# Optimization experiments

Measured on AMD Instinct MI355X. Metric: run time of the kernel, lower is better.

Reference implementation:

```python
import jax, jax.numpy as jnp
import numpy as np

M, N = 128, 128          # SOM grid
NITER = 1000             # total training iterations
ALPHA = 0.3              # base learning rate (torch default)
SIGMA = max(M, N) / 2.0  # base neighbourhood radius (torch default)
BS, DIM = 4096, 768


def setup_inputs() -> dict:
    key = jax.random.key(0)
    k1, k2 = jax.random.split(key)
    embedded = jax.random.normal(k1, (BS, DIM), dtype=jnp.float32)   # SapBERT CLS reps
    weights = jax.random.normal(k2, (M * N, DIM), dtype=jnp.float32)  # codebook / SOM weights
    return {"embedded": embedded, "weights": weights, "it": 100}


def reference(embedded, weights, it):
    comps = weights.shape[0]
    # neuron grid locations [comps, 2] (row-major i,j like neuron_locations())
    locs = jnp.stack(
        jnp.meshgrid(jnp.arange(M), jnp.arange(N), indexing="ij"), axis=-1
    ).reshape(comps, 2).astype(jnp.float32)

    # BMU search: squared Euclidean distances (argmin identical to argmin of sqrt)
    # [bs, comps] — avoids materializing the torch [bs, comps, dim] repeat
    d2 = (
        jnp.sum(embedded * embedded, axis=1)[:, None]
        + jnp.sum(weights * weights, axis=1)[None, :]
        - 2.0 * (embedded @ weights.T)
    )
    bmu_index = jnp.argmin(d2, axis=1)          # [bs]
    bmu_loc = locs[bmu_index]                   # [bs, 2] gather

    # linearly decaying learning rate / sigma
    decay = 1.0 - it / NITER
    alpha_op = ALPHA * decay
    sigma_op = SIGMA * decay

    # Gaussian neighbourhood over grid distances [bs, comps]
    grid_d2 = jnp.sum((locs[None, :, :] - bmu_loc[:, None, :]) ** 2, axis=-1)
    lr = alpha_op * jnp.exp(-grid_d2 / (sigma_op * sigma_op))

    # delta[c,d] = sum_b lr[b,c] * (x[b,d] - w[c,d])  (no bs x comps x dim materialization)
    delta = jnp.einsum("bc,bd->cd", lr, embedded) - jnp.sum(lr, axis=0)[:, None] * weights
    return weights + delta
```

## Files before the change

### kernel.cpp

```cpp
#include <hip/hip_runtime.h>
#include <cstdint>
#include <cstddef>

#define BS    4096
#define DIM   768
#define GM    128
#define GN    128
#define COMPS (GM * GN)
#define NITER_F 1000.0f
#define ALPHA0  0.3f
#define SIGMA0  64.0f

typedef _Float16 half8  __attribute__((ext_vector_type(8)));
typedef _Float16 half4v __attribute__((ext_vector_type(4)));
typedef _Float16 half2v __attribute__((ext_vector_type(2)));
typedef float    floatx4 __attribute__((ext_vector_type(4)));

#define XH_OFF    0UL
#define WH_OFF    (8UL * 1024UL * 1024UL)
#define G_OFF     0UL
#define G_BYTES   ((size_t)COMPS * DIM * 4UL)
#define BEST_OFF  G_BYTES
#define BEST_BYTES ((size_t)BS * 8UL)
#define CNT_OFF   (BEST_OFF + BEST_BYTES)
#define CNT_BYTES ((size_t)COMPS * 4UL)
#define CNTH_OFF  (CNT_OFF + CNT_BYTES)
#define S_OFF     (CNTH_OFF + CNT_BYTES)
#define WN2_OFF   (S_OFF + CNT_BYTES)

#define GPTR(p) ((const __attribute__((address_space(1))) void*)(p))
#define LPTR(p) ((__attribute__((address_space(3))) void*)(p))

__device__ __forceinline__ unsigned long long packScore(float s, int c) {
    unsigned u = __float_as_uint(s);
    u = (u & 0x80000000u) ? ~u : (u | 0x80000000u);
    return ((unsigned long long)u << 32) | (unsigned)(~(unsigned)c);
}

__device__ __forceinline__ unsigned long long shfl_xor_u64(unsigned long long v, int m) {
    unsigned lo = (unsigned)v, hi = (unsigned)(v >> 32);
    lo = (unsigned)__shfl_xor((int)lo, m, 64);
    hi = (unsigned)__shfl_xor((int)hi, m, 64);
    return ((unsigned long long)hi << 32) | lo;
}

__global__ void cvt_kernel(const float* __restrict__ src, _Float16* __restrict__ dst, int n4) {
    int i = blockIdx.x * 256 + threadIdx.x;
    if (i >= n4) return;
    float4 v = ((const float4*)src)[i];
    half4v h;
    h[0] = (_Float16)v.x; h[1] = (_Float16)v.y;
    h[2] = (_Float16)v.z; h[3] = (_Float16)v.w;
    ((half4v*)dst)[i] = h;
}

__global__ __launch_bounds__(192) void cvtw_wn2_kernel(
    const float* __restrict__ w, _Float16* __restrict__ wh, float* __restrict__ wn2) {
    const int c = blockIdx.x;
    const int t = threadIdx.x;
    const size_t i4 = (size_t)c * 192 + t;
    float4 v = ((const float4*)w)[i4];
    half4v h;
    h[0] = (_Float16)v.x; h[1] = (_Float16)v.y;
    h[2] = (_Float16)v.z; h[3] = (_Float16)v.w;
    ((half4v*)wh)[i4] = h;
    float s = v.x * v.x + v.y * v.y + v.z * v.z + v.w * v.w;
    #pragma unroll
    for (int off = 32; off; off >>= 1) s += __shfl_down(s, off, 64);
    __shared__ float p[3];
    if ((t & 63) == 0) p[t >> 6] = s;
    __syncthreads();
    if (t == 0) wn2[c] = 0.5f * (p[0] + p[1] + p[2]);
}

__global__ __launch_bounds__(256) void bmu_kernel(
    const _Float16* __restrict__ xh, const _Float16* __restrict__ wh,
    const float* __restrict__ wn2, unsigned long long* __restrict__ best) {
    __shared__ _Float16 xs[128 * 32];
    __shared__ _Float16 wsd[128 * 32];
    __shared__ unsigned long long red[128];

    const int tid  = threadIdx.x;
    const int wv   = tid >> 6;
    const int lane = tid & 63;
    const int c0 = blockIdx.x * 128;
    const int b0 = blockIdx.y * 128;

    if (tid < 128) red[tid] = 0ULL;

    floatx4 acc[4][4];
    #pragma unroll
    for (int i = 0; i < 4; ++i)
        #pragma unroll
        for (int j = 0; j < 4; ++j) acc[i][j] = (floatx4){0.f, 0.f, 0.f, 0.f};

    const int rr   = lane >> 2;
    const int pq   = lane & 3;
    const int kk   = pq ^ ((rr >> 1) & 3);
    const int lk   = kk * 8;
    const int q    = lane >> 4;
    const int l15  = lane & 15;
    const int mrow = (wv >> 1) * 64;
    const int ncol = (wv & 1) * 64;

    for (int k0 = 0; k0 < DIM; k0 += 32) {
        #pragma unroll
        for (int s = 0; s < 2; ++s) {
            const int sub = 2 * wv + s;
            const _Float16* gx = xh + (size_t)(b0 + sub * 16 + rr) * DIM + k0 + lk;
            __builtin_amdgcn_global_load_lds(GPTR(gx), LPTR(xs + sub * 512), 16, 0, 0);
            const _Float16* gw = wh + (size_t)(c0 + sub * 16 + rr) * DIM + k0 + lk;
            __builtin_amdgcn_global_load_lds(GPTR(gw), LPTR(wsd + sub * 512), 16, 0, 0);
        }
        __syncthreads();

        half8 af[4], bf[4];
        #pragma unroll
        for (int i = 0; i < 4; ++i) {
            const int row = mrow + i * 16 + l15;
            af[i] = *(const half8*)(xs + row * 32 + (q ^ ((row >> 1) & 3)) * 8);
        }
        #pragma unroll
        for (int j = 0; j < 4; ++j) {
            const int row = ncol + j * 16 + l15;
            bf[j] = *(const half8*)(wsd + row * 32 + (q ^ ((row >> 1) & 3)) * 8);
        }
        #pragma unroll
        for (int i = 0; i < 4; ++i)
            #pragma unroll
            for (int j = 0; j < 4; ++j)
                acc[i][j] = __builtin_amdgcn_mfma_f32_16x16x32_f16(af[i], bf[j], acc[i][j], 0, 0, 0);
        __syncthreads();
    }

    float wnj[4];
    #pragma unroll
    for (int j = 0; j < 4; ++j) wnj[j] = wn2[c0 + ncol + j * 16 + l15];

    #pragma unroll
    for (int i = 0; i < 4; ++i) {
        #pragma unroll
        for (int r = 0; r < 4; ++r) {
            unsigned long long m = 0ULL;
            #pragma unroll
            for (int j = 0; j < 4; ++j) {
                float s = acc[i][j][r] - wnj[j];
                unsigned long long p = packScore(s, c0 + ncol + j * 16 + l15);
                if (p > m) m = p;
            }
            #pragma unroll
            for (int msk = 1; msk <= 8; msk <<= 1) {
                unsigned long long o = shfl_xor_u64(m, msk);
                if (o > m) m = o;
            }
            if (l15 == 0)
                atomicMax(&red[mrow + i * 16 + q * 4 + r], m);
        }
    }
    __syncthreads();
    if (tid < 128) atomicMax(&best[b0 + tid], red[tid]);
}

__global__ void scatter_kernel(const unsigned long long* __restrict__ best,
                               const float* __restrict__ x,
                               float* __restrict__ G, float* __restrict__ cnt) {
    const int b = blockIdx.x;
    const int c = (int)(~(unsigned)(best[b] & 0xFFFFFFFFULL));
    float* gr = G + (size_t)c * DIM;
    const float* xr = x + (size_t)b * DIM;
    #pragma unroll
    for (int u = 0; u < 3; ++u) {
        const int d = threadIdx.x + u * 256;
        atomicAdd(&gr[d], xr[d]);
    }
    if (threadIdx.x == 0) atomicAdd(&cnt[c], 1.0f);
}

#define EP 136
#define BP 40

__global__ __launch_bounds__(256) void convA_kernel(
    const float* __restrict__ G, float* __restrict__ H, const int* __restrict__ itp) {
    __shared__ _Float16 Es[128 * EP];
    __shared__ _Float16 Bs[128 * BP];
    const int d0 = blockIdx.x * 128;
    const int ib = blockIdx.y;
    const int tid = threadIdx.x;
    const int wv = tid >> 6, lane = tid & 63;
    const int l15 = lane & 15, q = lane >> 4;
    const int mrow = (wv >> 1) * 64, ncol = (wv & 1) * 64;

    {
        const float decay = 1.f - (float)(*itp) / NITER_F;
        const float sig = SIGMA0 * decay;
        const float inv = -1.f / (sig * sig);
        const int row = tid >> 1, hh = tid & 1;
        _Float16* dst = Es + row * EP + hh * 64;
        #pragma unroll
        for (int u = 0; u < 64; ++u) {
            const float dd = (float)(row - hh * 64 - u);
            dst[u] = (_Float16)__expf(dd * dd * inv);
        }
    }

    floatx4 acc[4][4];
    #pragma unroll
    for (int i = 0; i < 4; ++i)
        #pragma unroll
        for (int j = 0; j < 4; ++j) acc[i][j] = (floatx4){0.f, 0.f, 0.f, 0.f};

    const int jj2 = (tid & 15) * 2;
    const int dd  = (tid >> 4) * 8;
    for (int k0 = 0; k0 < 128; k0 += 32) {
        __syncthreads();
        {
            const float* r0 = G + (size_t)(ib * 128 + k0 + jj2) * DIM + d0 + dd;
            const float* r1 = r0 + DIM;
            float4 a0 = *(const float4*)r0, a1 = *(const float4*)(r0 + 4);
            float4 b0 = *(const float4*)r1, b1 = *(const float4*)(r1 + 4);
            float va[8] = {a0.x, a0.y, a0.z, a0.w, a1.x, a1.y, a1.z, a1.w};
            float vb[8] = {b0.x, b0.y, b0.z, b0.w, b1.x, b1.y, b1.z, b1.w};
            #pragma unroll
            for (int u = 0; u < 8; ++u)
                *(half2v*)(Bs + (dd + u) * BP + jj2) = (half2v){(_Float16)va[u], (_Float16)vb[u]};
        }
        __syncthreads();
        half8 af[4], bf[4];
        #pragma unroll
        for (int i = 0; i < 4; ++i)
            af[i] = *(const half8*)(Es + (mrow + i * 16 + l15) * EP + k0 + q * 8);
        #pragma unroll
        for (int j = 0; j < 4; ++j)
            bf[j] = *(const half8*)(Bs + (ncol + j * 16 + l15) * BP + q * 8);
        #pragma unroll
        for (int i = 0; i < 4; ++i)
            #pragma unroll
            for (int j = 0; j < 4; ++j)
                acc[i][j] = __builtin_amdgcn_mfma_f32_16x16x32_f16(af[i], bf[j], acc[i][j], 0, 0, 0);
    }
    __syncthreads();
    float* Ebf = (float*)Es;
    #pragma unroll
    for (int ch = 0; ch < 2; ++ch) {
        if ((wv >> 1) == ch) {
            #pragma unroll
            for (int i = 0; i < 4; ++i)
                #pragma unroll
                for (int j = 0; j < 4; ++j)
                    #pragma unroll
                    for (int r = 0; r < 4; ++r)
                        Ebf[(i * 16 + q * 4 + r) * 132 + ncol + j * 16 + l15] = acc[i][j][r];
        }
        __syncthreads();
        {
            const int row = tid >> 2, seg = tid & 3;
            const int m = ch * 64 + row;
            const size_t g = (size_t)(ib * 128 + m) * DIM + d0 + seg * 32;
            #pragma unroll
            for (int u = 0; u < 8; ++u)
                *(float4*)(H + g + u * 4) = *(const float4*)(Ebf + row * 132 + seg * 32 + u * 4);
        }
        __syncthreads();
    }
}

__global__ __launch_bounds__(256) void convB_kernel(
    const float* H, const float* __restrict__ w,
    const float* __restrict__ S, const int* __restrict__ itp, float* out) {
    __shared__ _Float16 Es[128 * EP];
    __shared__ _Float16 Bs[128 * BP];
    const int d0 = blockIdx.x * 128;
    const int jc = blockIdx.y;
    const int tid = threadIdx.x;
    const int wv = tid >> 6, lane = tid & 63;
    const int l15 = lane & 15, q = lane >> 4;
    const int mrow = (wv >> 1) * 64, ncol = (wv & 1) * 64;
    const float alpha = ALPHA0 * (1.f - (float)(*itp) / NITER_F);

    {
        const float decay = 1.f - (float)(*itp) / NITER_F;
        const float sig = SIGMA0 * decay;
        const float inv = -1.f / (sig * sig);
        const int row = tid >> 1, hh = tid & 1;
        _Float16* dst = Es + row * EP + hh * 64;
        #pragma unroll
        for (int u = 0; u < 64; ++u) {
            const float dd = (float)(row - hh * 64 - u);
            dst[u] = (_Float16)__expf(dd * dd * inv);
        }
    }

    floatx4 acc[4][4];
    #pragma unroll
    for (int i = 0; i < 4; ++i)
        #pragma unroll
        for (int j = 0; j < 4; ++j) acc[i][j] = (floatx4){0.f, 0.f, 0.f, 0.f};

    const int jj2 = (tid & 15) * 2;
    const int dd  = (tid >> 4) * 8;
    for (int k0 = 0; k0 < 128; k0 += 32) {
        __syncthreads();
        {
            const float* r0 = H + (size_t)((k0 + jj2) * 128 + jc) * DIM + d0 + dd;
            const float* r1 = r0 + (size_t)128 * DIM;
            float4 a0 = *(const float4*)r0, a1 = *(const float4*)(r0 + 4);
            float4 b0 = *(const float4*)r1, b1 = *(const float4*)(r1 + 4);
            float va[8] = {a0.x, a0.y, a0.z, a0.w, a1.x, a1.y, a1.z, a1.w};
            float vb[8] = {b0.x, b0.y, b0.z, b0.w, b1.x, b1.y, b1.z, b1.w};
            #pragma unroll
            for (int u = 0; u < 8; ++u)
                *(half2v*)(Bs + (dd + u) * BP + jj2) = (half2v){(_Float16)va[u], (_Float16)vb[u]};
        }
        __syncthreads();
        half8 af[4], bf[4];
        #pragma unroll
        for (int i = 0; i < 4; ++i)
            af[i] = *(const half8*)(Es + (mrow + i * 16 + l15) * EP + k0 + q * 8);
        #pragma unroll
        for (int j = 0; j < 4; ++j)
            bf[j] = *(const half8*)(Bs + (ncol + j * 16 + l15) * BP + q * 8);
        #pragma unroll
        for (int i = 0; i < 4; ++i)
            #pragma unroll
            for (int j = 0; j < 4; ++j)
                acc[i][j] = __builtin_amdgcn_mfma_f32_16x16x32_f16(af[i], bf[j], acc[i][j], 0, 0, 0);
    }
    __syncthreads();
    float* Ebf = (float*)Es;
    #pragma unroll
    for (int ch = 0; ch < 2; ++ch) {
        if ((wv >> 1) == ch) {
            #pragma unroll
            for (int i = 0; i < 4; ++i)
                #pragma unroll
                for (int j = 0; j < 4; ++j)
                    #pragma unroll
                    for (int r = 0; r < 4; ++r)
                        Ebf[(i * 16 + q * 4 + r) * 132 + ncol + j * 16 + l15] = acc[i][j][r];
        }
        __syncthreads();
        {
            const int row = tid >> 2, seg = tid & 3;
            const int m = ch * 64 + row;
            const int c = m * 128 + jc;
            const float scl = 1.f - alpha * S[c];
            const size_t g = (size_t)c * DIM + d0 + seg * 32;
            #pragma unroll
            for (int u = 0; u < 8; ++u) {
                float4 wv4 = *(const float4*)(w + g + u * 4);
                float4 t4  = *(const float4*)(Ebf + row * 132 + seg * 32 + u * 4);
                float4 o;
                o.x = wv4.x * scl + alpha * t4.x;
                o.y = wv4.y * scl + alpha * t4.y;
                o.z = wv4.z * scl + alpha * t4.z;
                o.w = wv4.w * scl + alpha * t4.w;
                *(float4*)(out + g + u * 4) = o;
            }
        }
        __syncthreads();
    }
}

__global__ void cntconv1(const float* __restrict__ cnt, float* __restrict__ cntH,
                         const int* __restrict__ itp) {
    const int idx = blockIdx.x * 256 + threadIdx.x;
    const int i = idx >> 7, jc = idx & 127;
    const float decay = 1.f - (float)(*itp) / NITER_F;
    const float sig = SIGMA0 * decay;
    const float inv = -1.f / (sig * sig);
    float s = 0.f;
    for (int j = 0; j < 128; ++j) {
        const float dd = (float)(jc - j);
        s += __expf(dd * dd * inv) * cnt[i * 128 + j];
    }
    cntH[idx] = s;
}
__global__ void cntconv2(const float* __restrict__ cntH, float* __restrict__ S,
                         const int* __restrict__ itp) {
    const int idx = blockIdx.x * 256 + threadIdx.x;
    const int ic = idx >> 7, jc = idx & 127;
    const float decay = 1.f - (float)(*itp) / NITER_F;
    const float sig = SIGMA0 * decay;
    const float inv = -1.f / (sig * sig);
    float s = 0.f;
    for (int i = 0; i < 128; ++i) {
        const float dd = (float)(ic - i);
        s += __expf(dd * dd * inv) * cntH[i * 128 + jc];
    }
    S[idx] = s;
}

extern "C" void kernel_launch(void* const* d_in, const int* in_sizes, int n_in,
                              void* d_out, int out_size, void* d_ws, size_t ws_size,
                              hipStream_t stream) {
    const float* x  = (const float*)d_in[0];
    const float* w  = (const float*)d_in[1];
    const int* itp  = (const int*)d_in[2];
    float* out = (float*)d_out;
    char* ws = (char*)d_ws;

    _Float16* xh = (_Float16*)(ws + XH_OFF);
    _Float16* wh = (_Float16*)(ws + WH_OFF);
    float*    G  = (float*)(ws + G_OFF);
    unsigned long long* best = (unsigned long long*)(ws + BEST_OFF);
    float* cnt  = (float*)(ws + CNT_OFF);
    float* cntH = (float*)(ws + CNTH_OFF);
    float* S    = (float*)(ws + S_OFF);
    float* wn2  = (float*)(ws + WN2_OFF);

    hipMemsetAsync(ws + BEST_OFF, 0, BEST_BYTES + CNT_BYTES, stream);

    cvt_kernel<<<(BS * DIM / 4 + 255) / 256, 256, 0, stream>>>(x, xh, BS * DIM / 4);
    cvtw_wn2_kernel<<<COMPS, 192, 0, stream>>>(w, wh, wn2);

    bmu_kernel<<<dim3(COMPS / 128, BS / 128), 256, 0, stream>>>(xh, wh, wn2, best);

    hipMemsetAsync(ws + G_OFF, 0, G_BYTES, stream);
    scatter_kernel<<<BS, 256, 0, stream>>>(best, x, G, cnt);

    cntconv1<<<COMPS / 256, 256, 0, stream>>>(cnt, cntH, itp);
    cntconv2<<<COMPS / 256, 256, 0, stream>>>(cntH, S, itp);

    convA_kernel<<<dim3(6, 128), 256, 0, stream>>>(G, out, itp);
    convB_kernel<<<dim3(6, 128), 256, 0, stream>>>(out, w, S, itp, out);
}
```

Before: 346.9 us.

## Widen BMU K-tile, store intermediate as fp16 in-place, fuse count convolutions into convB

The BMU GEMM now stages 64-wide K tiles with an 8-way XOR swizzle, which halves the number of barrier pairs. convA writes its intermediate H as fp16 into the G buffer, interleaved per row, instead of fp32 into the output, cutting that traffic roughly in half. The two separable count-convolution kernels are removed, and each convB block now computes its 128 S values in shared memory. The cost is redundant exp work in every convB block (each of the 768 blocks recomputes its column's count convolution) and a risk of the in-place fp16 H overwriting G rows that another block still reads.

```diff
diff --git a/kernel.cpp b/kernel.cpp
--- a/kernel.cpp
+++ b/kernel.cpp
@@ -13,7 +13,6 @@
 
 typedef _Float16 half8  __attribute__((ext_vector_type(8)));
 typedef _Float16 half4v __attribute__((ext_vector_type(4)));
-typedef _Float16 half2v __attribute__((ext_vector_type(2)));
 typedef float    floatx4 __attribute__((ext_vector_type(4)));
 
 #define XH_OFF    0UL
@@ -24,9 +23,7 @@
 #define BEST_BYTES ((size_t)BS * 8UL)
 #define CNT_OFF   (BEST_OFF + BEST_BYTES)
 #define CNT_BYTES ((size_t)COMPS * 4UL)
-#define CNTH_OFF  (CNT_OFF + CNT_BYTES)
-#define S_OFF     (CNTH_OFF + CNT_BYTES)
-#define WN2_OFF   (S_OFF + CNT_BYTES)
+#define WN2_OFF   (CNT_OFF + CNT_BYTES)
 
 #define GPTR(p) ((const __attribute__((address_space(1))) void*)(p))
 #define LPTR(p) ((__attribute__((address_space(3))) void*)(p))
@@ -76,8 +73,8 @@
 __global__ __launch_bounds__(256) void bmu_kernel(
     const _Float16* __restrict__ xh, const _Float16* __restrict__ wh,
     const float* __restrict__ wn2, unsigned long long* __restrict__ best) {
-    __shared__ _Float16 xs[128 * 32];
-    __shared__ _Float16 wsd[128 * 32];
+    __shared__ _Float16 xs[128 * 64];
+    __shared__ _Float16 wsd[128 * 64];
     __shared__ unsigned long long red[128];
 
     const int tid  = threadIdx.x;
@@ -94,42 +91,47 @@
         #pragma unroll
         for (int j = 0; j < 4; ++j) acc[i][j] = (floatx4){0.f, 0.f, 0.f, 0.f};
 
-    const int rr   = lane >> 2;
-    const int pq   = lane & 3;
-    const int kk   = pq ^ ((rr >> 1) & 3);
-    const int lk   = kk * 8;
+    const int srow = lane >> 3;
+    const int spos = lane & 7;
     const int q    = lane >> 4;
     const int l15  = lane & 15;
     const int mrow = (wv >> 1) * 64;
     const int ncol = (wv & 1) * 64;
 
-    for (int k0 = 0; k0 < DIM; k0 += 32) {
-        #pragma unroll
-        for (int s = 0; s < 2; ++s) {
-            const int sub = 2 * wv + s;
-            const _Float16* gx = xh + (size_t)(b0 + sub * 16 + rr) * DIM + k0 + lk;
-            __builtin_amdgcn_global_load_lds(GPTR(gx), LPTR(xs + sub * 512), 16, 0, 0);
-            const _Float16* gw = wh + (size_t)(c0 + sub * 16 + rr) * DIM + k0 + lk;
-            __builtin_amdgcn_global_load_lds(GPTR(gw), LPTR(wsd + sub * 512), 16, 0, 0);
-        }
-        __syncthreads();
-
-        half8 af[4], bf[4];
-        #pragma unroll
-        for (int i = 0; i < 4; ++i) {
-            const int row = mrow + i * 16 + l15;
-            af[i] = *(const half8*)(xs + row * 32 + (q ^ ((row >> 1) & 3)) * 8);
-        }
-        #pragma unroll
-        for (int j = 0; j < 4; ++j) {
-            const int row = ncol + j * 16 + l15;
-            bf[j] = *(const half8*)(wsd + row * 32 + (q ^ ((row >> 1) & 3)) * 8);
-        }
-        #pragma unroll
-        for (int i = 0; i < 4; ++i)
-            #pragma unroll
-            for (int j = 0; j < 4; ++j)
-                acc[i][j] = __builtin_amdgcn_mfma_f32_16x16x32_f16(af[i], bf[j], acc[i][j], 0, 0, 0);
+    for (int k0 = 0; k0 < DIM; k0 += 64) {
+        #pragma unroll
+        for (int s = 0; s < 4; ++s) {
+            const int rbase = wv * 32 + s * 8;
+            const int row = rbase + srow;
+            const int kk = spos ^ (row & 7);
+            const _Float16* gx = xh + (size_t)(b0 + row) * DIM + k0 + kk * 8;
+            __builtin_amdgcn_global_load_lds(GPTR(gx), LPTR(xs + rbase * 64), 16, 0, 0);
+            const _Float16* gw = wh + (size_t)(c0 + row) * DIM + k0 + kk * 8;
+            __builtin_amdgcn_global_load_lds(GPTR(gw), LPTR(wsd + rbase * 64), 16, 0, 0);
+        }
+        __syncthreads();
+
+        #pragma unroll
+        for (int h = 0; h < 2; ++h) {
+            half8 af[4], bf[4];
+            #pragma unroll
+            for (int i = 0; i < 4; ++i) {
+                const int row = mrow + i * 16 + l15;
+                const int ck = (h * 4 + q) ^ (row & 7);
+                af[i] = *(const half8*)(xs + row * 64 + ck * 8);
+            }
+            #pragma unroll
+            for (int j = 0; j < 4; ++j) {
+                const int row = ncol + j * 16 + l15;
+                const int ck = (h * 4 + q) ^ (row & 7);
+                bf[j] = *(const half8*)(wsd + row * 64 + ck * 8);
+            }
+            #pragma unroll
+            for (int i = 0; i < 4; ++i)
+                #pragma unroll
+                for (int j = 0; j < 4; ++j)
+                    acc[i][j] = __builtin_amdgcn_mfma_f32_16x16x32_f16(af[i], bf[j], acc[i][j], 0, 0, 0);
+        }
         __syncthreads();
     }
 
@@ -180,7 +182,7 @@
 #define BP 40
 
 __global__ __launch_bounds__(256) void convA_kernel(
-    const float* __restrict__ G, float* __restrict__ H, const int* __restrict__ itp) {
+    const float* G, _Float16* Hh, const int* __restrict__ itp) {
     __shared__ _Float16 Es[128 * EP];
     __shared__ _Float16 Bs[128 * BP];
     const int d0 = blockIdx.x * 128;
@@ -209,20 +211,19 @@
         #pragma unroll
         for (int j = 0; j < 4; ++j) acc[i][j] = (floatx4){0.f, 0.f, 0.f, 0.f};
 
-    const int jj2 = (tid & 15) * 2;
-    const int dd  = (tid >> 4) * 8;
+    const int dpo = (tid & 15) * 8;
+    const int rsel = tid >> 4;
     for (int k0 = 0; k0 < 128; k0 += 32) {
         __syncthreads();
-        {
-            const float* r0 = G + (size_t)(ib * 128 + k0 + jj2) * DIM + d0 + dd;
-            const float* r1 = r0 + DIM;
-            float4 a0 = *(const float4*)r0, a1 = *(const float4*)(r0 + 4);
-            float4 b0 = *(const float4*)r1, b1 = *(const float4*)(r1 + 4);
+        #pragma unroll
+        for (int s = 0; s < 2; ++s) {
+            const int j = k0 + s * 16 + rsel;
+            const float* r = G + (size_t)(ib * 128 + j) * DIM + d0 + dpo;
+            float4 a0 = *(const float4*)r, a1 = *(const float4*)(r + 4);
             float va[8] = {a0.x, a0.y, a0.z, a0.w, a1.x, a1.y, a1.z, a1.w};
-            float vb[8] = {b0.x, b0.y, b0.z, b0.w, b1.x, b1.y, b1.z, b1.w};
             #pragma unroll
             for (int u = 0; u < 8; ++u)
-                *(half2v*)(Bs + (dd + u) * BP + jj2) = (half2v){(_Float16)va[u], (_Float16)vb[u]};
+                Bs[(dpo + u) * BP + (s * 16 + rsel)] = (_Float16)va[u];
         }
         __syncthreads();
         half8 af[4], bf[4];
@@ -255,32 +256,47 @@
         {
             const int row = tid >> 2, seg = tid & 3;
             const int m = ch * 64 + row;
-            const size_t g = (size_t)(ib * 128 + m) * DIM + d0 + seg * 32;
-            #pragma unroll
-            for (int u = 0; u < 8; ++u)
-                *(float4*)(H + g + u * 4) = *(const float4*)(Ebf + row * 132 + seg * 32 + u * 4);
+            _Float16* hp = Hh + (size_t)(ib * 128 + m) * 1536 + d0 * 2 + seg * 32;
+            #pragma unroll
+            for (int u = 0; u < 4; ++u) {
+                const float* sp = Ebf + row * 132 + seg * 32 + u * 8;
+                half8 hv;
+                #pragma unroll
+                for (int e = 0; e < 8; ++e) hv[e] = (_Float16)sp[e];
+                *(half8*)(hp + u * 8) = hv;
+            }
         }
         __syncthreads();
     }
 }
 
 __global__ __launch_bounds__(256) void convB_kernel(
-    const float* H, const float* __restrict__ w,
-    const float* __restrict__ S, const int* __restrict__ itp, float* out) {
+    const _Float16* Hh, const float* __restrict__ w, const float* __restrict__ cnt,
+    const int* __restrict__ itp, float* __restrict__ out) {
     __shared__ _Float16 Es[128 * EP];
     __shared__ _Float16 Bs[128 * BP];
+    __shared__ float cntHs[128];
+    __shared__ float Ss[128];
     const int d0 = blockIdx.x * 128;
     const int jc = blockIdx.y;
     const int tid = threadIdx.x;
     const int wv = tid >> 6, lane = tid & 63;
     const int l15 = lane & 15, q = lane >> 4;
     const int mrow = (wv >> 1) * 64, ncol = (wv & 1) * 64;
-    const float alpha = ALPHA0 * (1.f - (float)(*itp) / NITER_F);
-
+    const float decay = 1.f - (float)(*itp) / NITER_F;
+    const float alpha = ALPHA0 * decay;
+    const float sig = SIGMA0 * decay;
+    const float inv = -1.f / (sig * sig);
+
+    if (tid < 128) {
+        float s = 0.f;
+        for (int j = 0; j < 128; ++j) {
+            const float dd = (float)(jc - j);
+            s += __expf(dd * dd * inv) * cnt[tid * 128 + j];
+        }
+        cntHs[tid] = s;
+    }
     {
-        const float decay = 1.f - (float)(*itp) / NITER_F;
-        const float sig = SIGMA0 * decay;
-        const float inv = -1.f / (sig * sig);
         const int row = tid >> 1, hh = tid & 1;
         _Float16* dst = Es + row * EP + hh * 64;
         #pragma unroll
@@ -289,6 +305,15 @@
             dst[u] = (_Float16)__expf(dd * dd * inv);
         }
     }
+    __syncthreads();
+    if (tid < 128) {
+        float s = 0.f;
+        for (int i = 0; i < 128; ++i) {
+            const float dd = (float)(tid - i);
+            s += __expf(dd * dd * inv) * cntHs[i];
+        }
+        Ss[tid] = s;
+    }
 
     floatx4 acc[4][4];
     #pragma unroll
@@ -296,20 +321,17 @@
         #pragma unroll
         for (int j = 0; j < 4; ++j) acc[i][j] = (floatx4){0.f, 0.f, 0.f, 0.f};
 
-    const int jj2 = (tid & 15) * 2;
-    const int dd  = (tid >> 4) * 8;
+    const int dpo = (tid & 15) * 8;
+    const int rsel = tid >> 4;
     for (int k0 = 0; k0 < 128; k0 += 32) {
         __syncthreads();
-        {
-            const float* r0 = H + (size_t)((k0 + jj2) * 128 + jc) * DIM + d0 + dd;
-            const float* r1 = r0 + (size_t)128 * DIM;
-            float4 a0 = *(const float4*)r0, a1 = *(const float4*)(r0 + 4);
-            float4 b0 = *(const float4*)r1, b1 = *(const float4*)(r1 + 4);
-            float va[8] = {a0.x, a0.y, a0.z, a0.w, a1.x, a1.y, a1.z, a1.w};
-            float vb[8] = {b0.x, b0.y, b0.z, b0.w, b1.x, b1.y, b1.z, b1.w};
+        #pragma unroll
+        for (int s = 0; s < 2; ++s) {
+            const int i = k0 + s * 16 + rsel;
+            const half8 v = *(const half8*)(Hh + (size_t)(i * 128 + jc) * 1536 + d0 * 2 + dpo);
             #pragma unroll
             for (int u = 0; u < 8; ++u)
-                *(half2v*)(Bs + (dd + u) * BP + jj2) = (half2v){(_Float16)va[u], (_Float16)vb[u]};
+                Bs[(dpo + u) * BP + (s * 16 + rsel)] = v[u];
         }
         __syncthreads();
         half8 af[4], bf[4];
@@ -343,7 +365,7 @@
             const int row = tid >> 2, seg = tid & 3;
             const int m = ch * 64 + row;
             const int c = m * 128 + jc;
-            const float scl = 1.f - alpha * S[c];
+            const float scl = 1.f - alpha * Ss[m];
             const size_t g = (size_t)c * DIM + d0 + seg * 32;
             #pragma unroll
             for (int u = 0; u < 8; ++u) {
@@ -361,35 +383,6 @@
     }
 }
 
-__global__ void cntconv1(const float* __restrict__ cnt, float* __restrict__ cntH,
-                         const int* __restrict__ itp) {
-    const int idx = blockIdx.x * 256 + threadIdx.x;
-    const int i = idx >> 7, jc = idx & 127;
-    const float decay = 1.f - (float)(*itp) / NITER_F;
-    const float sig = SIGMA0 * decay;
-    const float inv = -1.f / (sig * sig);
-    float s = 0.f;
-    for (int j = 0; j < 128; ++j) {
-        const float dd = (float)(jc - j);
-        s += __expf(dd * dd * inv) * cnt[i * 128 + j];
-    }
-    cntH[idx] = s;
-}
-__global__ void cntconv2(const float* __restrict__ cntH, float* __restrict__ S,
-                         const int* __restrict__ itp) {
-    const int idx = blockIdx.x * 256 + threadIdx.x;
-    const int ic = idx >> 7, jc = idx & 127;
-    const float decay = 1.f - (float)(*itp) / NITER_F;
-    const float sig = SIGMA0 * decay;
-    const float inv = -1.f / (sig * sig);
-    float s = 0.f;
-    for (int i = 0; i < 128; ++i) {
-        const float dd = (float)(ic - i);
-        s += __expf(dd * dd * inv) * cntH[i * 128 + jc];
-    }
-    S[idx] = s;
-}
-
 extern "C" void kernel_launch(void* const* d_in, const int* in_sizes, int n_in,
                               void* d_out, int out_size, void* d_ws, size_t ws_size,
                               hipStream_t stream) {
@@ -402,10 +395,9 @@
     _Float16* xh = (_Float16*)(ws + XH_OFF);
     _Float16* wh = (_Float16*)(ws + WH_OFF);
     float*    G  = (float*)(ws + G_OFF);
+    _Float16* Hh = (_Float16*)(ws + G_OFF);
     unsigned long long* best = (unsigned long long*)(ws + BEST_OFF);
     float* cnt  = (float*)(ws + CNT_OFF);
-    float* cntH = (float*)(ws + CNTH_OFF);
-    float* S    = (float*)(ws + S_OFF);
     float* wn2  = (float*)(ws + WN2_OFF);
 
     hipMemsetAsync(ws + BEST_OFF, 0, BEST_BYTES + CNT_BYTES, stream);
@@ -418,9 +410,6 @@
     hipMemsetAsync(ws + G_OFF, 0, G_BYTES, stream);
     scatter_kernel<<<BS, 256, 0, stream>>>(best, x, G, cnt);
 
-    cntconv1<<<COMPS / 256, 256, 0, stream>>>(cnt, cntH, itp);
-    cntconv2<<<COMPS / 256, 256, 0, stream>>>(cntH, S, itp);
-
-    convA_kernel<<<dim3(6, 128), 256, 0, stream>>>(G, out, itp);
-    convB_kernel<<<dim3(6, 128), 256, 0, stream>>>(out, w, S, itp, out);
-}
+    convA_kernel<<<dim3(6, 128), 256, 0, stream>>>(G, Hh, itp);
+    convB_kernel<<<dim3(6, 128), 256, 0, stream>>>(Hh, w, cnt, itp, out);
+}
```

New measurement: 345.2 us. About the same (-0.5%).
